# Optimization experiments

Measured on AMD Instinct MI355X. Metric: run time of the kernel, lower is better.

The kernel has to match this reference:

```python
import jax, jax.numpy as jnp
import numpy as np

DIM = 384
HEADS = 12
WH, WW = 7, 7
N = WH * WW
NW = 64          # windows per image
B_ = 4096        # total windows (64 images * 64 windows)


def _relative_position_index():
    ch = np.arange(WH)
    cw = np.arange(WW)
    coords = np.stack(np.meshgrid(ch, cw, indexing='ij'))          # 2, Wh, Ww
    cf = coords.reshape(2, -1)                                     # 2, N
    rel = cf[:, :, None] - cf[:, None, :]                          # 2, N, N
    rel = rel.transpose(1, 2, 0).copy()                            # N, N, 2
    rel[:, :, 0] += WH - 1
    rel[:, :, 1] += WW - 1
    rel[:, :, 0] *= 2 * WW - 1
    return rel.sum(-1).astype(np.int32)                            # N, N


def setup_inputs() -> dict:
    key = jax.random.key(0)
    ks = jax.random.split(key, 7)
    x = jax.random.normal(ks[0], (B_, N, DIM), dtype=jnp.float32)
    mask = jax.random.normal(ks[1], (NW, N, N), dtype=jnp.float32)
    qkv_w = jax.random.normal(ks[2], (3 * DIM, DIM), dtype=jnp.float32) * 0.02
    qkv_b = jax.random.normal(ks[3], (3 * DIM,), dtype=jnp.float32) * 0.02
    proj_w = jax.random.normal(ks[4], (DIM, DIM), dtype=jnp.float32) * 0.02
    proj_b = jax.random.normal(ks[5], (DIM,), dtype=jnp.float32) * 0.02
    bias_table = jax.random.normal(ks[6], (169, HEADS), dtype=jnp.float32) * 0.02
    rel_idx = jnp.asarray(_relative_position_index())
    return {"x": x, "mask": mask, "qkv_w": qkv_w, "qkv_b": qkv_b,
            "proj_w": proj_w, "proj_b": proj_b, "bias_table": bias_table,
            "rel_idx": rel_idx}


def reference(x, mask, qkv_w, qkv_b, proj_w, proj_b, bias_table, rel_idx):
    B, Nn, C = x.shape
    hd = C // HEADS
    scale = hd ** (-0.5)
    # qkv projection: (B, N, 3C) -> (3, B, H, N, hd)
    qkv = (x @ qkv_w.T + qkv_b).reshape(B, Nn, 3, HEADS, hd).transpose(2, 0, 3, 1, 4)
    q, k, v = qkv[0], qkv[1], qkv[2]
    attn = jnp.einsum('bhnd,bhmd->bhnm', q * scale, k)             # B, H, N, N
    # gathered relative-position bias: (N, N, H) -> (H, N, N)
    bias = bias_table[rel_idx.reshape(-1)].reshape(Nn, Nn, HEADS).transpose(2, 0, 1)
    attn = attn + bias[None]
    nW = mask.shape[0]
    attn = attn.reshape(B // nW, nW, HEADS, Nn, Nn) + mask[None, :, None]
    attn = attn.reshape(B, HEADS, Nn, Nn)
    attn = jax.nn.softmax(attn, axis=-1)
    out = jnp.einsum('bhnm,bhmd->bnhd', attn, v).reshape(B, Nn, C)
    return out @ proj_w.T + proj_b
```

## Files before the change

### kernel.cpp

```cpp
#include <hip/hip_runtime.h>


#define NTOK 49
#define DIM 384
#define HEADS 12
#define QKV_OC 1152
#define QKV_ELEMS (1152*384)
#define PROJ_ELEMS (384*384)
#define CMB_ELEMS (64*12*49*49)
#define SCALE 0.17677669529663687f

typedef __attribute__((ext_vector_type(8))) __bf16 bf16x8;
typedef __attribute__((ext_vector_type(4))) float f32x4;

union BF8 { bf16x8 v; unsigned short u[8]; uint4 q; };

#define GLOAD_LDS16(gp, lp)                                                  \
  __builtin_amdgcn_global_load_lds(                                          \
      (const __attribute__((address_space(1))) void*)(gp),                   \
      (__attribute__((address_space(3))) void*)(lp), 16, 0, 0)

__device__ __forceinline__ unsigned short f2bf(float f) {
  union { float f; unsigned u; } x; x.f = f;
  unsigned r = x.u + 0x7fffu + ((x.u >> 16) & 1u);
  return (unsigned short)(r >> 16);
}

__device__ __forceinline__ bf16x8 zbf8() {
  BF8 z;
  #pragma unroll
  for (int j = 0; j < 8; ++j) z.u[j] = 0;
  return z.v;
}

__global__ void prep_kernel(const float* __restrict__ qkv_w,
                            const float* __restrict__ proj_w,
                            const float* __restrict__ bias_table,
                            const int* __restrict__ rel_idx,
                            const float* __restrict__ mask,
                            const float* __restrict__ qkv_b,
                            unsigned short* __restrict__ wq,
                            unsigned short* __restrict__ wp,
                            float* __restrict__ cmb,
                            float* __restrict__ qb2) {
  int i = blockIdx.x * 256 + threadIdx.x;
  if (i < QKV_ELEMS) {
    int c = i / 384, j = i % 384, s = j >> 3, e = j & 7;
    float v = qkv_w[c * 384 + ((s ^ (c & 7)) << 3) + e];
    if (c < 384) v *= SCALE;
    wq[i] = f2bf(v);
  } else if (i < QKV_ELEMS + PROJ_ELEMS) {
    int k = i - QKV_ELEMS;
    int c = k / 384, j = k % 384, s = j >> 3, e = j & 7;
    wp[k] = f2bf(proj_w[c * 384 + ((s ^ (c & 7)) << 3) + e]);
  } else if (i < QKV_ELEMS + PROJ_ELEMS + CMB_ELEMS) {
    int j = i - QKV_ELEMS - PROJ_ELEMS;
    int row = j % 49;
    int tok = (j / 49) % 49;
    int h   = (j / 2401) % 12;
    int wi  = j / (2401 * 12);
    cmb[j] = bias_table[rel_idx[row * 49 + tok] * HEADS + h]
           + mask[(wi * 49 + row) * 49 + tok];
  } else if (i < QKV_ELEMS + PROJ_ELEMS + CMB_ELEMS + QKV_OC) {
    int c = i - QKV_ELEMS - PROJ_ELEMS - CMB_ELEMS;
    qb2[c] = qkv_b[c] * (c < 384 ? SCALE : 1.0f);
  }
}

__global__ void convx_kernel(const float* __restrict__ x,
                             unsigned short* __restrict__ xsw, long ngran) {
  long gidx = (long)blockIdx.x * 256 + threadIdx.x;
  if (gidx >= ngran) return;
  int r = (int)(gidx / 48), s = (int)(gidx % 48);
  int ssrc = (s & 56) | ((s & 7) ^ (r & 7));
  const float* src = x + (size_t)r * 384 + ssrc * 8;
  float4 f0 = *(const float4*)src;
  float4 f1 = *(const float4*)(src + 4);
  BF8 t;
  t.u[0] = f2bf(f0.x); t.u[1] = f2bf(f0.y); t.u[2] = f2bf(f0.z); t.u[3] = f2bf(f0.w);
  t.u[4] = f2bf(f1.x); t.u[5] = f2bf(f1.y); t.u[6] = f2bf(f1.z); t.u[7] = f2bf(f1.w);
  *(uint4*)(xsw + (size_t)r * 384 + s * 8) = t.q;
}

template<int BF16OUT>
__global__ __launch_bounds__(256, 4) void gemm128(
    const unsigned short* __restrict__ Asw, const unsigned short* __restrict__ Wsw,
    const float* __restrict__ bias, void* __restrict__ Cout,
    int Mrows, int Ntot, int ncp) {
  __shared__ alignas(16) unsigned short As[128 * 64];
  __shared__ alignas(16) unsigned short Bs[128 * 64];
  const int nwg = gridDim.x;
  const int bid = blockIdx.x;
  const int q8 = nwg >> 3, r8 = nwg & 7;
  const int xcd = bid & 7, lin = bid >> 3;
  const int wgid = (xcd < r8 ? xcd * (q8 + 1) : r8 * (q8 + 1) + (xcd - r8) * q8) + lin;
  const int colp = wgid % ncp, rowb = wgid / ncp;
  const int tb = rowb * 128, nb = colp * 128;
  const int tid = threadIdx.x;
  const int wave = tid >> 6, lane = tid & 63, g = lane >> 4, li = lane & 15;
  const int wr = wave >> 1, wc = wave & 1;
  const int chbase = wave * 256 + lane;

  f32x4 acc[4][4];
  #pragma unroll
  for (int m = 0; m < 4; ++m)
    #pragma unroll
    for (int n = 0; n < 4; ++n) acc[m][n] = (f32x4){0.f, 0.f, 0.f, 0.f};

  #pragma unroll 1
  for (int step = 0; step < 6; ++step) {
    const int k0 = step * 64;
    if (step) __syncthreads();
    #pragma unroll
    for (int i = 0; i < 4; ++i) {
      int ch = chbase + i * 64;
      int r = ch >> 3, s = ch & 7;
      GLOAD_LDS16(Asw + (size_t)(tb + r) * 384 + k0 + s * 8,
                  (unsigned short*)As + ch * 8);
    }
    #pragma unroll
    for (int i = 0; i < 4; ++i) {
      int ch = chbase + i * 64;
      int c = ch >> 3, s = ch & 7;
      GLOAD_LDS16(Wsw + (size_t)(nb + c) * 384 + k0 + s * 8,
                  (unsigned short*)Bs + ch * 8);
    }
    __syncthreads();

    #pragma unroll
    for (int kk = 0; kk < 2; ++kk) {
      const int goff = ((kk * 4 + g) ^ (li & 7)) << 3;
      bf16x8 a0 = *(const bf16x8*)&As[(wr * 64 +  0 + li) * 64 + goff];
      bf16x8 a1 = *(const bf16x8*)&As[(wr * 64 + 16 + li) * 64 + goff];
      bf16x8 a2 = *(const bf16x8*)&As[(wr * 64 + 32 + li) * 64 + goff];
      bf16x8 a3 = *(const bf16x8*)&As[(wr * 64 + 48 + li) * 64 + goff];
      bf16x8 b0 = *(const bf16x8*)&Bs[(wc * 64 +  0 + li) * 64 + goff];
      bf16x8 b1 = *(const bf16x8*)&Bs[(wc * 64 + 16 + li) * 64 + goff];
      bf16x8 b2 = *(const bf16x8*)&Bs[(wc * 64 + 32 + li) * 64 + goff];
      bf16x8 b3 = *(const bf16x8*)&Bs[(wc * 64 + 48 + li) * 64 + goff];
      acc[0][0] = __builtin_amdgcn_mfma_f32_16x16x32_bf16(a0, b0, acc[0][0], 0, 0, 0);
      acc[0][1] = __builtin_amdgcn_mfma_f32_16x16x32_bf16(a0, b1, acc[0][1], 0, 0, 0);
      acc[0][2] = __builtin_amdgcn_mfma_f32_16x16x32_bf16(a0, b2, acc[0][2], 0, 0, 0);
      acc[0][3] = __builtin_amdgcn_mfma_f32_16x16x32_bf16(a0, b3, acc[0][3], 0, 0, 0);
      acc[1][0] = __builtin_amdgcn_mfma_f32_16x16x32_bf16(a1, b0, acc[1][0], 0, 0, 0);
      acc[1][1] = __builtin_amdgcn_mfma_f32_16x16x32_bf16(a1, b1, acc[1][1], 0, 0, 0);
      acc[1][2] = __builtin_amdgcn_mfma_f32_16x16x32_bf16(a1, b2, acc[1][2], 0, 0, 0);
      acc[1][3] = __builtin_amdgcn_mfma_f32_16x16x32_bf16(a1, b3, acc[1][3], 0, 0, 0);
      acc[2][0] = __builtin_amdgcn_mfma_f32_16x16x32_bf16(a2, b0, acc[2][0], 0, 0, 0);
      acc[2][1] = __builtin_amdgcn_mfma_f32_16x16x32_bf16(a2, b1, acc[2][1], 0, 0, 0);
      acc[2][2] = __builtin_amdgcn_mfma_f32_16x16x32_bf16(a2, b2, acc[2][2], 0, 0, 0);
      acc[2][3] = __builtin_amdgcn_mfma_f32_16x16x32_bf16(a2, b3, acc[2][3], 0, 0, 0);
      acc[3][0] = __builtin_amdgcn_mfma_f32_16x16x32_bf16(a3, b0, acc[3][0], 0, 0, 0);
      acc[3][1] = __builtin_amdgcn_mfma_f32_16x16x32_bf16(a3, b1, acc[3][1], 0, 0, 0);
      acc[3][2] = __builtin_amdgcn_mfma_f32_16x16x32_bf16(a3, b2, acc[3][2], 0, 0, 0);
      acc[3][3] = __builtin_amdgcn_mfma_f32_16x16x32_bf16(a3, b3, acc[3][3], 0, 0, 0);
    }
  }

  #pragma unroll
  for (int n = 0; n < 4; ++n) {
    int col = nb + wc * 64 + n * 16 + li;
    float bv = bias[col];
    #pragma unroll
    for (int m = 0; m < 4; ++m) {
      #pragma unroll
      for (int r4 = 0; r4 < 4; ++r4) {
        int row = tb + wr * 64 + m * 16 + g * 4 + r4;
        if (row < Mrows) {
          float v = acc[m][n][r4] + bv;
          if (BF16OUT) ((unsigned short*)Cout)[(size_t)row * Ntot + col] = f2bf(v);
          else         ((float*)Cout)[(size_t)row * Ntot + col] = v;
        }
      }
    }
  }
}

#define AT_K 0
#define AT_V (49*128)
#define AT_ELEMS (AT_V + 49*138)

__global__ __launch_bounds__(512, 6) void attn_kernel(
    const unsigned short* __restrict__ qkv,
    const float* __restrict__ cmb,
    unsigned short* __restrict__ Obuf,
    int wb0) {
  __shared__ unsigned short lds[AT_ELEMS];
  const int tid  = threadIdx.x;
  const int wave = tid >> 6, lane = tid & 63;
  const int g = lane >> 4, li = lane & 15;
  const int relw = blockIdx.x;
  const int wi = (wb0 + relw) & 63;
  const size_t rowbase = (size_t)relw * 49;
  const int mgrp = wave >> 1, ng = wave & 1;
  const int arow = mgrp * 16 + li;

  #pragma unroll 1
  for (int c = 0; c < 3; ++c) {
    if (c) __syncthreads();
    #pragma unroll
    for (int it = 0; it < 2; ++it) {
      int gidx = it * 512 + tid;
      if (gidx < 784) {
        int row = gidx >> 4, gc = gidx & 15;
        bf16x8 v = *(const bf16x8*)(qkv + (rowbase + row) * 1152 + 384 + c * 128 + gc * 8);
        *(bf16x8*)&lds[AT_K + row * 128 + ((gc ^ (row & 7)) << 3)] = v;
      }
    }
    #pragma unroll
    for (int it = 0; it < 2; ++it) {
      int gidx = it * 512 + tid;
      if (gidx < 784) {
        int row = gidx >> 4, gc = gidx & 15;
        BF8 v;
        v.q = *(const uint4*)(qkv + (rowbase + row) * 1152 + 768 + c * 128 + gc * 8);
        int e = AT_V + row * 138 + gc * 8;
        *(unsigned*)&lds[e]     = v.q.x;
        *(unsigned*)&lds[e + 2] = v.q.y;
        *(unsigned*)&lds[e + 4] = v.q.z;
        *(unsigned*)&lds[e + 6] = v.q.w;
      }
    }
    __syncthreads();

    #pragma unroll 1
    for (int b = 0; b < 2; ++b) {
      const int hh = ng * 2 + b;
      const int h  = c * 4 + hh;

      bf16x8 qa = (arow < NTOK)
          ? *(const bf16x8*)(qkv + (rowbase + arow) * 1152 + h * 32 + g * 8)
          : zbf8();

      f32x4 sv[4];
      #pragma unroll
      for (int nt = 0; nt < 4; ++nt) {
        int tok = nt * 16 + li;
        bf16x8 kf = (tok < NTOK)
            ? *(const bf16x8*)&lds[AT_K + tok * 128 + (((hh * 4 + g) ^ (tok & 7)) << 3)]
            : zbf8();
        f32x4 z4 = (f32x4){0.f, 0.f, 0.f, 0.f};
        sv[nt] = __builtin_amdgcn_mfma_f32_16x16x32_bf16(kf, qa, z4, 0, 0, 0);
      }

      const float* cb = cmb + (size_t)(wi * HEADS + h) * (NTOK * NTOK);
      #pragma unroll
      for (int nt = 0; nt < 4; ++nt) {
        #pragma unroll
        for (int r4 = 0; r4 < 4; ++r4) {
          int tok = nt * 16 + g * 4 + r4;
          float v;
          if (tok < NTOK) {
            v = sv[nt][r4];
            if (arow < NTOK) v += cb[tok * NTOK + arow];
          } else {
            v = -1e30f;
          }
          sv[nt][r4] = v;
        }
      }

      float m = -1e30f;
      #pragma unroll
      for (int nt = 0; nt < 4; ++nt)
        #pragma unroll
        for (int r4 = 0; r4 < 4; ++r4) m = fmaxf(m, sv[nt][r4]);
      m = fmaxf(m, __shfl_xor(m, 16));
      m = fmaxf(m, __shfl_xor(m, 32));
      float s = 0.f;
      #pragma unroll
      for (int nt = 0; nt < 4; ++nt)
        #pragma unroll
        for (int r4 = 0; r4 < 4; ++r4) {
          float e = __expf(sv[nt][r4] - m);
          sv[nt][r4] = e;
          s += e;
        }
      s += __shfl_xor(s, 16);
      s += __shfl_xor(s, 32);
      float inv = 1.f / s;
      #pragma unroll
      for (int nt = 0; nt < 4; ++nt)
        #pragma unroll
        for (int r4 = 0; r4 < 4; ++r4) sv[nt][r4] *= inv;

      bf16x8 pa[2];
      #pragma unroll
      for (int k2 = 0; k2 < 2; ++k2) {
        BF8 pf;
        #pragma unroll
        for (int j = 0; j < 8; ++j) {
          int srcLane = (((g * 2 + (j >> 2)) & 3) << 4) | li;
          float v0 = __shfl(sv[k2 * 2][j & 3], srcLane);
          float v1 = __shfl(sv[k2 * 2 + 1][j & 3], srcLane);
          pf.u[j] = f2bf((g >= 2) ? v1 : v0);
        }
        pa[k2] = pf.v;
      }

      f32x4 oa[2];
      oa[0] = (f32x4){0.f, 0.f, 0.f, 0.f};
      oa[1] = (f32x4){0.f, 0.f, 0.f, 0.f};
      #pragma unroll
      for (int k2 = 0; k2 < 2; ++k2) {
        #pragma unroll
        for (int nt2 = 0; nt2 < 2; ++nt2) {
          BF8 vb;
          int ch = hh * 32 + nt2 * 16 + li;
          #pragma unroll
          for (int j = 0; j < 8; ++j) {
            int tok = k2 * 32 + g * 8 + j;
            vb.u[j] = (tok < NTOK) ? lds[AT_V + tok * 138 + ch] : (unsigned short)0;
          }
          oa[nt2] = __builtin_amdgcn_mfma_f32_16x16x32_bf16(pa[k2], vb.v, oa[nt2], 0, 0, 0);
        }
      }

      #pragma unroll
      for (int nt2 = 0; nt2 < 2; ++nt2) {
        int colb = h * 32 + nt2 * 16 + li;
        int gran = colb >> 3;
        #pragma unroll
        for (int r4 = 0; r4 < 4; ++r4) {
          int row = mgrp * 16 + g * 4 + r4;
          if (row < NTOK) {
            int grow = (int)(rowbase) + row;
            int col2 = (((gran & 56) | ((gran & 7) ^ (grow & 7))) << 3) | (colb & 7);
            Obuf[(size_t)grow * 384 + col2] = f2bf(oa[nt2][r4]);
          }
        }
      }
    }
  }
}

extern "C" void kernel_launch(void* const* d_in, const int* in_sizes, int n_in,
                              void* d_out, int out_size, void* d_ws, size_t ws_size,
                              hipStream_t stream) {
  (void)in_sizes; (void)n_in; (void)out_size;
  const float* x          = (const float*)d_in[0];
  const float* mask       = (const float*)d_in[1];
  const float* qkv_w      = (const float*)d_in[2];
  const float* qkv_b      = (const float*)d_in[3];
  const float* proj_w     = (const float*)d_in[4];
  const float* proj_b     = (const float*)d_in[5];
  const float* bias_table = (const float*)d_in[6];
  const int*   rel_idx    = (const int*)d_in[7];
  float* out = (float*)d_out;

  char* ws = (char*)d_ws;
  size_t off = 0;
  unsigned short* wq  = (unsigned short*)(ws + off); off += (size_t)QKV_ELEMS * 2;
  unsigned short* wp  = (unsigned short*)(ws + off); off += (size_t)PROJ_ELEMS * 2;
  float*          qb2 = (float*)(ws + off);          off += (size_t)QKV_OC * 4;
  float*          cmb = (float*)(ws + off);          off += (size_t)CMB_ELEMS * 4;
  const size_t fixed = off;

  const int cands[7] = {2048, 4096, 1024, 512, 256, 128, 64};
  int WB = 64;
  for (int ci = 0; ci < 7; ++ci) {
    int mrows = cands[ci] * 49;
    int mpad = ((mrows + 127) / 128) * 128;
    size_t need = fixed + (size_t)mpad * 384 * 2 + (size_t)mrows * 1152 * 2;
    if (need <= ws_size) { WB = cands[ci]; break; }
  }
  const int Mrows = WB * 49;
  const int Mpad  = ((Mrows + 127) / 128) * 128;
  const int NRB   = Mpad / 128;
  unsigned short* xsw = (unsigned short*)(ws + fixed);
  unsigned short* qkv = xsw + (size_t)Mpad * 384;

  const int prep_total = QKV_ELEMS + PROJ_ELEMS + CMB_ELEMS + QKV_OC;
  prep_kernel<<<(prep_total + 255) / 256, 256, 0, stream>>>(
      qkv_w, proj_w, bias_table, rel_idx, mask, qkv_b, wq, wp, cmb, qb2);

  const int NB = 4096 / WB;
  const long ngran = (long)Mrows * 48;
  for (int b = 0; b < NB; ++b) {
    convx_kernel<<<(int)((ngran + 255) / 256), 256, 0, stream>>>(
        x + (size_t)b * Mrows * 384, xsw, ngran);
    gemm128<1><<<NRB * 9, 256, 0, stream>>>(xsw, wq, qb2, (void*)qkv,
                                            Mrows, 1152, 9);
    attn_kernel<<<WB, 512, 0, stream>>>(qkv, cmb, xsw, b * WB);
    gemm128<0><<<NRB * 3, 256, 0, stream>>>(xsw, wp, proj_b,
        (void*)(out + (size_t)b * Mrows * 384), Mrows, 384, 3);
  }
}
```

Baseline: 1.050 ms.

## Transpose V in LDS for vector reads and stage bf16 GEMM epilogue through LDS

The attention kernel now stores V transposed and XOR-swizzled in LDS, with the padding tokens zeroed. Each MFMA B-fragment then comes from one 16-byte LDS read instead of eight scalar 16-bit loads with bounds checks. The bf16-output GEMM epilogue writes results into a swizzled LDS tile and stores full rows with 16-byte global writes, replacing scattered 2-byte stores. Occupancy hints are raised on both kernels. Risk: the V zero-fill happens before the first barrier while other waves may already be writing V data into the same region, so it could race.

Result: slower. 1.217 ms (+15.9%).

```diff
diff --git a/kernel.cpp b/kernel.cpp
--- a/kernel.cpp
+++ b/kernel.cpp
@@ -83,12 +83,13 @@
 }
 
 template<int BF16OUT>
-__global__ __launch_bounds__(256, 4) void gemm128(
+__global__ __launch_bounds__(256, 5) void gemm128(
     const unsigned short* __restrict__ Asw, const unsigned short* __restrict__ Wsw,
     const float* __restrict__ bias, void* __restrict__ Cout,
     int Mrows, int Ntot, int ncp) {
-  __shared__ alignas(16) unsigned short As[128 * 64];
-  __shared__ alignas(16) unsigned short Bs[128 * 64];
+  __shared__ alignas(16) unsigned short Buf[16384];
+  unsigned short* As = Buf;
+  unsigned short* Bs = Buf + 8192;
   const int nwg = gridDim.x;
   const int bid = blockIdx.x;
   const int q8 = nwg >> 3, r8 = nwg & 7;
@@ -115,15 +116,13 @@
     for (int i = 0; i < 4; ++i) {
       int ch = chbase + i * 64;
       int r = ch >> 3, s = ch & 7;
-      GLOAD_LDS16(Asw + (size_t)(tb + r) * 384 + k0 + s * 8,
-                  (unsigned short*)As + ch * 8);
+      GLOAD_LDS16(Asw + (size_t)(tb + r) * 384 + k0 + s * 8, As + ch * 8);
     }
     #pragma unroll
     for (int i = 0; i < 4; ++i) {
       int ch = chbase + i * 64;
       int c = ch >> 3, s = ch & 7;
-      GLOAD_LDS16(Wsw + (size_t)(nb + c) * 384 + k0 + s * 8,
-                  (unsigned short*)Bs + ch * 8);
+      GLOAD_LDS16(Wsw + (size_t)(nb + c) * 384 + k0 + s * 8, Bs + ch * 8);
     }
     __syncthreads();
 
@@ -157,19 +156,44 @@
     }
   }
 
-  #pragma unroll
-  for (int n = 0; n < 4; ++n) {
-    int col = nb + wc * 64 + n * 16 + li;
-    float bv = bias[col];
-    #pragma unroll
-    for (int m = 0; m < 4; ++m) {
-      #pragma unroll
-      for (int r4 = 0; r4 < 4; ++r4) {
-        int row = tb + wr * 64 + m * 16 + g * 4 + r4;
-        if (row < Mrows) {
-          float v = acc[m][n][r4] + bv;
-          if (BF16OUT) ((unsigned short*)Cout)[(size_t)row * Ntot + col] = f2bf(v);
-          else         ((float*)Cout)[(size_t)row * Ntot + col] = v;
+  if (BF16OUT) {
+    __syncthreads();
+    #pragma unroll
+    for (int n = 0; n < 4; ++n) {
+      int colL = wc * 64 + n * 16 + li;
+      float bv = bias[nb + colL];
+      int gg = colL >> 3, ge = colL & 7;
+      #pragma unroll
+      for (int m = 0; m < 4; ++m) {
+        #pragma unroll
+        for (int r4 = 0; r4 < 4; ++r4) {
+          int row = wr * 64 + m * 16 + g * 4 + r4;
+          Buf[row * 128 + ((gg ^ (row & 7)) << 3) + ge] = f2bf(acc[m][n][r4] + bv);
+        }
+      }
+    }
+    __syncthreads();
+    const int row = tid >> 1, half = tid & 1;
+    if (tb + row < Mrows) {
+      unsigned short* dst = (unsigned short*)Cout + (size_t)(tb + row) * Ntot + nb + half * 64;
+      #pragma unroll
+      for (int i = 0; i < 8; ++i) {
+        int gg = half * 8 + i;
+        *(uint4*)(dst + i * 8) = *(const uint4*)&Buf[row * 128 + ((gg ^ (row & 7)) << 3)];
+      }
+    }
+  } else {
+    #pragma unroll
+    for (int n = 0; n < 4; ++n) {
+      int col = nb + wc * 64 + n * 16 + li;
+      float bv = bias[col];
+      #pragma unroll
+      for (int m = 0; m < 4; ++m) {
+        #pragma unroll
+        for (int r4 = 0; r4 < 4; ++r4) {
+          int row = tb + wr * 64 + m * 16 + g * 4 + r4;
+          if (row < Mrows)
+            ((float*)Cout)[(size_t)row * Ntot + col] = acc[m][n][r4] + bv;
         }
       }
     }
@@ -177,10 +201,10 @@
 }
 
 #define AT_K 0
-#define AT_V (49*128)
-#define AT_ELEMS (AT_V + 49*138)
-
-__global__ __launch_bounds__(512, 6) void attn_kernel(
+#define AT_VT (49*128)
+#define AT_ELEMS (AT_VT + 128*64)
+
+__global__ __launch_bounds__(512, 8) void attn_kernel(
     const unsigned short* __restrict__ qkv,
     const float* __restrict__ cmb,
     unsigned short* __restrict__ Obuf,
@@ -195,6 +219,13 @@
   const int mgrp = wave >> 1, ng = wave & 1;
   const int arow = mgrp * 16 + li;
 
+  {
+    uint4 z4 = {0u, 0u, 0u, 0u};
+    uint4* p = (uint4*)(lds + AT_VT);
+    p[tid] = z4;
+    p[tid + 512] = z4;
+  }
+
   #pragma unroll 1
   for (int c = 0; c < 3; ++c) {
     if (c) __syncthreads();
@@ -214,11 +245,11 @@
         int row = gidx >> 4, gc = gidx & 15;
         BF8 v;
         v.q = *(const uint4*)(qkv + (rowbase + row) * 1152 + 768 + c * 128 + gc * 8);
-        int e = AT_V + row * 138 + gc * 8;
-        *(unsigned*)&lds[e]     = v.q.x;
-        *(unsigned*)&lds[e + 2] = v.q.y;
-        *(unsigned*)&lds[e + 4] = v.q.z;
-        *(unsigned*)&lds[e + 6] = v.q.w;
+        #pragma unroll
+        for (int e = 0; e < 8; ++e) {
+          int ch = gc * 8 + e;
+          lds[AT_VT + ch * 64 + (row ^ (e << 3))] = v.u[e];
+        }
       }
     }
     __syncthreads();
@@ -305,14 +336,10 @@
       for (int k2 = 0; k2 < 2; ++k2) {
         #pragma unroll
         for (int nt2 = 0; nt2 < 2; ++nt2) {
-          BF8 vb;
           int ch = hh * 32 + nt2 * 16 + li;
-          #pragma unroll
-          for (int j = 0; j < 8; ++j) {
-            int tok = k2 * 32 + g * 8 + j;
-            vb.u[j] = (tok < NTOK) ? lds[AT_V + tok * 138 + ch] : (unsigned short)0;
-          }
-          oa[nt2] = __builtin_amdgcn_mfma_f32_16x16x32_bf16(pa[k2], vb.v, oa[nt2], 0, 0, 0);
+          int tg = k2 * 4 + g;
+          bf16x8 vb = *(const bf16x8*)&lds[AT_VT + ch * 64 + ((tg ^ (ch & 7)) << 3)];
+          oa[nt2] = __builtin_amdgcn_mfma_f32_16x16x32_bf16(pa[k2], vb, oa[nt2], 0, 0, 0);
         }
       }
 
```

## Double-buffer GEMM LDS tiles with K=32 stages and 4-granule swizzle

Applied to the files above, without the earlier changes.

The 128x128 GEMM now uses two 128x32 LDS buffers per operand and prefetches the next K-stage with global_load_lds while MFMAs run on the current stage, instead of loading a 64-wide K slice and then computing. The XOR swizzle changes from 8-granule to 4-granule groups to fit the 32-wide rows, and every producer and consumer (weight prep, x conversion, attention output write) is updated to match. The workspace candidate order now prefers a single batch of 4096 windows, meaning fewer launches but a larger workspace. In exchange, a barrier now sits after every 32-wide K step, twelve per tile instead of six.

Result: slower. 1.073 ms (+2.2%).

```diff
diff --git a/kernel.cpp b/kernel.cpp
--- a/kernel.cpp
+++ b/kernel.cpp
@@ -31,6 +31,10 @@
   #pragma unroll
   for (int j = 0; j < 8; ++j) z.u[j] = 0;
   return z.v;
+}
+
+__device__ __forceinline__ int swz4(int s, int c) {
+  return (s & ~3) | ((s & 3) ^ ((c >> 1) & 3));
 }
 
 __global__ void prep_kernel(const float* __restrict__ qkv_w,
@@ -46,13 +50,13 @@
   int i = blockIdx.x * 256 + threadIdx.x;
   if (i < QKV_ELEMS) {
     int c = i / 384, j = i % 384, s = j >> 3, e = j & 7;
-    float v = qkv_w[c * 384 + ((s ^ (c & 7)) << 3) + e];
+    float v = qkv_w[c * 384 + swz4(s, c) * 8 + e];
     if (c < 384) v *= SCALE;
     wq[i] = f2bf(v);
   } else if (i < QKV_ELEMS + PROJ_ELEMS) {
     int k = i - QKV_ELEMS;
     int c = k / 384, j = k % 384, s = j >> 3, e = j & 7;
-    wp[k] = f2bf(proj_w[c * 384 + ((s ^ (c & 7)) << 3) + e]);
+    wp[k] = f2bf(proj_w[c * 384 + swz4(s, c) * 8 + e]);
   } else if (i < QKV_ELEMS + PROJ_ELEMS + CMB_ELEMS) {
     int j = i - QKV_ELEMS - PROJ_ELEMS;
     int row = j % 49;
@@ -72,8 +76,7 @@
   long gidx = (long)blockIdx.x * 256 + threadIdx.x;
   if (gidx >= ngran) return;
   int r = (int)(gidx / 48), s = (int)(gidx % 48);
-  int ssrc = (s & 56) | ((s & 7) ^ (r & 7));
-  const float* src = x + (size_t)r * 384 + ssrc * 8;
+  const float* src = x + (size_t)r * 384 + swz4(s, r) * 8;
   float4 f0 = *(const float4*)src;
   float4 f1 = *(const float4*)(src + 4);
   BF8 t;
@@ -87,8 +90,8 @@
     const unsigned short* __restrict__ Asw, const unsigned short* __restrict__ Wsw,
     const float* __restrict__ bias, void* __restrict__ Cout,
     int Mrows, int Ntot, int ncp) {
-  __shared__ alignas(16) unsigned short As[128 * 64];
-  __shared__ alignas(16) unsigned short Bs[128 * 64];
+  __shared__ alignas(16) unsigned short As[2][128 * 32];
+  __shared__ alignas(16) unsigned short Bs[2][128 * 32];
   const int nwg = gridDim.x;
   const int bid = blockIdx.x;
   const int q8 = nwg >> 3, r8 = nwg & 7;
@@ -99,7 +102,7 @@
   const int tid = threadIdx.x;
   const int wave = tid >> 6, lane = tid & 63, g = lane >> 4, li = lane & 15;
   const int wr = wave >> 1, wc = wave & 1;
-  const int chbase = wave * 256 + lane;
+  const int chbase = wave * 128 + lane;
 
   f32x4 acc[4][4];
   #pragma unroll
@@ -107,54 +110,59 @@
     #pragma unroll
     for (int n = 0; n < 4; ++n) acc[m][n] = (f32x4){0.f, 0.f, 0.f, 0.f};
 
+  auto stage = [&](int bu, int st) {
+    const int k0 = st * 32;
+    #pragma unroll
+    for (int i = 0; i < 2; ++i) {
+      int ch = chbase + i * 64;
+      int r = ch >> 2, s = ch & 3;
+      GLOAD_LDS16(Asw + (size_t)(tb + r) * 384 + k0 + s * 8,
+                  (unsigned short*)As[bu] + ch * 8);
+    }
+    #pragma unroll
+    for (int i = 0; i < 2; ++i) {
+      int ch = chbase + i * 64;
+      int c = ch >> 2, s = ch & 3;
+      GLOAD_LDS16(Wsw + (size_t)(nb + c) * 384 + k0 + s * 8,
+                  (unsigned short*)Bs[bu] + ch * 8);
+    }
+  };
+
+  stage(0, 0);
+  __syncthreads();
+
   #pragma unroll 1
-  for (int step = 0; step < 6; ++step) {
-    const int k0 = step * 64;
-    if (step) __syncthreads();
-    #pragma unroll
-    for (int i = 0; i < 4; ++i) {
-      int ch = chbase + i * 64;
-      int r = ch >> 3, s = ch & 7;
-      GLOAD_LDS16(Asw + (size_t)(tb + r) * 384 + k0 + s * 8,
-                  (unsigned short*)As + ch * 8);
-    }
-    #pragma unroll
-    for (int i = 0; i < 4; ++i) {
-      int ch = chbase + i * 64;
-      int c = ch >> 3, s = ch & 7;
-      GLOAD_LDS16(Wsw + (size_t)(nb + c) * 384 + k0 + s * 8,
-                  (unsigned short*)Bs + ch * 8);
-    }
+  for (int st = 0; st < 12; ++st) {
+    const int cur = st & 1;
+    if (st + 1 < 12) stage(cur ^ 1, st + 1);
+
+    const int goff = ((g ^ ((li >> 1) & 3)) << 3);
+    bf16x8 a0 = *(const bf16x8*)&As[cur][(wr * 64 +  0 + li) * 32 + goff];
+    bf16x8 a1 = *(const bf16x8*)&As[cur][(wr * 64 + 16 + li) * 32 + goff];
+    bf16x8 a2 = *(const bf16x8*)&As[cur][(wr * 64 + 32 + li) * 32 + goff];
+    bf16x8 a3 = *(const bf16x8*)&As[cur][(wr * 64 + 48 + li) * 32 + goff];
+    bf16x8 b0 = *(const bf16x8*)&Bs[cur][(wc * 64 +  0 + li) * 32 + goff];
+    bf16x8 b1 = *(const bf16x8*)&Bs[cur][(wc * 64 + 16 + li) * 32 + goff];
+    bf16x8 b2 = *(const bf16x8*)&Bs[cur][(wc * 64 + 32 + li) * 32 + goff];
+    bf16x8 b3 = *(const bf16x8*)&Bs[cur][(wc * 64 + 48 + li) * 32 + goff];
+    acc[0][0] = __builtin_amdgcn_mfma_f32_16x16x32_bf16(a0, b0, acc[0][0], 0, 0, 0);
+    acc[0][1] = __builtin_amdgcn_mfma_f32_16x16x32_bf16(a0, b1, acc[0][1], 0, 0, 0);
+    acc[0][2] = __builtin_amdgcn_mfma_f32_16x16x32_bf16(a0, b2, acc[0][2], 0, 0, 0);
+    acc[0][3] = __builtin_amdgcn_mfma_f32_16x16x32_bf16(a0, b3, acc[0][3], 0, 0, 0);
+    acc[1][0] = __builtin_amdgcn_mfma_f32_16x16x32_bf16(a1, b0, acc[1][0], 0, 0, 0);
+    acc[1][1] = __builtin_amdgcn_mfma_f32_16x16x32_bf16(a1, b1, acc[1][1], 0, 0, 0);
+    acc[1][2] = __builtin_amdgcn_mfma_f32_16x16x32_bf16(a1, b2, acc[1][2], 0, 0, 0);
+    acc[1][3] = __builtin_amdgcn_mfma_f32_16x16x32_bf16(a1, b3, acc[1][3], 0, 0, 0);
+    acc[2][0] = __builtin_amdgcn_mfma_f32_16x16x32_bf16(a2, b0, acc[2][0], 0, 0, 0);
+    acc[2][1] = __builtin_amdgcn_mfma_f32_16x16x32_bf16(a2, b1, acc[2][1], 0, 0, 0);
+    acc[2][2] = __builtin_amdgcn_mfma_f32_16x16x32_bf16(a2, b2, acc[2][2], 0, 0, 0);
+    acc[2][3] = __builtin_amdgcn_mfma_f32_16x16x32_bf16(a2, b3, acc[2][3], 0, 0, 0);
+    acc[3][0] = __builtin_amdgcn_mfma_f32_16x16x32_bf16(a3, b0, acc[3][0], 0, 0, 0);
+    acc[3][1] = __builtin_amdgcn_mfma_f32_16x16x32_bf16(a3, b1, acc[3][1], 0, 0, 0);
+    acc[3][2] = __builtin_amdgcn_mfma_f32_16x16x32_bf16(a3, b2, acc[3][2], 0, 0, 0);
+    acc[3][3] = __builtin_amdgcn_mfma_f32_16x16x32_bf16(a3, b3, acc[3][3], 0, 0, 0);
+
     __syncthreads();
-
-    #pragma unroll
-    for (int kk = 0; kk < 2; ++kk) {
-      const int goff = ((kk * 4 + g) ^ (li & 7)) << 3;
-      bf16x8 a0 = *(const bf16x8*)&As[(wr * 64 +  0 + li) * 64 + goff];
-      bf16x8 a1 = *(const bf16x8*)&As[(wr * 64 + 16 + li) * 64 + goff];
-      bf16x8 a2 = *(const bf16x8*)&As[(wr * 64 + 32 + li) * 64 + goff];
-      bf16x8 a3 = *(const bf16x8*)&As[(wr * 64 + 48 + li) * 64 + goff];
-      bf16x8 b0 = *(const bf16x8*)&Bs[(wc * 64 +  0 + li) * 64 + goff];
-      bf16x8 b1 = *(const bf16x8*)&Bs[(wc * 64 + 16 + li) * 64 + goff];
-      bf16x8 b2 = *(const bf16x8*)&Bs[(wc * 64 + 32 + li) * 64 + goff];
-      bf16x8 b3 = *(const bf16x8*)&Bs[(wc * 64 + 48 + li) * 64 + goff];
-      acc[0][0] = __builtin_amdgcn_mfma_f32_16x16x32_bf16(a0, b0, acc[0][0], 0, 0, 0);
-      acc[0][1] = __builtin_amdgcn_mfma_f32_16x16x32_bf16(a0, b1, acc[0][1], 0, 0, 0);
-      acc[0][2] = __builtin_amdgcn_mfma_f32_16x16x32_bf16(a0, b2, acc[0][2], 0, 0, 0);
-      acc[0][3] = __builtin_amdgcn_mfma_f32_16x16x32_bf16(a0, b3, acc[0][3], 0, 0, 0);
-      acc[1][0] = __builtin_amdgcn_mfma_f32_16x16x32_bf16(a1, b0, acc[1][0], 0, 0, 0);
-      acc[1][1] = __builtin_amdgcn_mfma_f32_16x16x32_bf16(a1, b1, acc[1][1], 0, 0, 0);
-      acc[1][2] = __builtin_amdgcn_mfma_f32_16x16x32_bf16(a1, b2, acc[1][2], 0, 0, 0);
-      acc[1][3] = __builtin_amdgcn_mfma_f32_16x16x32_bf16(a1, b3, acc[1][3], 0, 0, 0);
-      acc[2][0] = __builtin_amdgcn_mfma_f32_16x16x32_bf16(a2, b0, acc[2][0], 0, 0, 0);
-      acc[2][1] = __builtin_amdgcn_mfma_f32_16x16x32_bf16(a2, b1, acc[2][1], 0, 0, 0);
-      acc[2][2] = __builtin_amdgcn_mfma_f32_16x16x32_bf16(a2, b2, acc[2][2], 0, 0, 0);
-      acc[2][3] = __builtin_amdgcn_mfma_f32_16x16x32_bf16(a2, b3, acc[2][3], 0, 0, 0);
-      acc[3][0] = __builtin_amdgcn_mfma_f32_16x16x32_bf16(a3, b0, acc[3][0], 0, 0, 0);
-      acc[3][1] = __builtin_amdgcn_mfma_f32_16x16x32_bf16(a3, b1, acc[3][1], 0, 0, 0);
-      acc[3][2] = __builtin_amdgcn_mfma_f32_16x16x32_bf16(a3, b2, acc[3][2], 0, 0, 0);
-      acc[3][3] = __builtin_amdgcn_mfma_f32_16x16x32_bf16(a3, b3, acc[3][3], 0, 0, 0);
-    }
   }
 
   #pragma unroll
@@ -325,8 +333,8 @@
           int row = mgrp * 16 + g * 4 + r4;
           if (row < NTOK) {
             int grow = (int)(rowbase) + row;
-            int col2 = (((gran & 56) | ((gran & 7) ^ (grow & 7))) << 3) | (colb & 7);
-            Obuf[(size_t)grow * 384 + col2] = f2bf(oa[nt2][r4]);
+            int pos = swz4(gran, grow);
+            Obuf[(size_t)grow * 384 + (pos << 3) + (colb & 7)] = f2bf(oa[nt2][r4]);
           }
         }
       }
@@ -356,7 +364,7 @@
   float*          cmb = (float*)(ws + off);          off += (size_t)CMB_ELEMS * 4;
   const size_t fixed = off;
 
-  const int cands[7] = {2048, 4096, 1024, 512, 256, 128, 64};
+  const int cands[7] = {4096, 2048, 1024, 512, 256, 128, 64};
   int WB = 64;
   for (int ci = 0; ci < 7; ++ci) {
     int mrows = cands[ci] * 49;
```
